# Kernel tuning notes

Measured on AMD Instinct MI355X. Metric: run time of the kernel, lower is better.

The kernel has to match this reference:

```python
import jax, jax.numpy as jnp
import numpy as np

HIDDEN = 2048
HEAD_DIM = 128
Q_HEAD = 16
KV_HEAD = 2
MAX_TOKEN = 4096
THETA = 10000
B = 1
S = 2048
SCALER = 1.0 / np.sqrt(HEAD_DIM)


def make_pos_emb():
    # Faithful port of ROPEEmbedding.create_embedding
    i = np.repeat(np.arange(HEAD_DIM // 2), 2)            # [D]
    freq = np.power(float(THETA), -i * 2.0 / HEAD_DIM)    # [D]
    t = np.einsum('i,j->ij', freq, np.arange(MAX_TOKEN, dtype=np.float64))  # [D, T]
    cos = np.cos(t)
    sin = np.sin(t)
    sin[0::2] *= -1.0                                      # negate even rows (even dim indices)
    pe = np.concatenate([cos, sin], axis=0).T              # [T, 2D]
    return jnp.asarray(pe, jnp.float32)


def _flip_pairs(x):
    # swap adjacent pairs along last dim: (x0,x1,x2,x3,..) -> (x1,x0,x3,x2,..)
    b, h, s, d = x.shape
    return x.reshape(b, h, s, d // 2, 2)[..., ::-1].reshape(b, h, s, d)


def _apply_rope(x, pos_emb):
    # x: [B, H, S, D]; pos_emb: [max_token, 2D]
    s = x.shape[2]
    pe = pos_emb[:s]                     # [S, 2D]
    cos = pe[:, :HEAD_DIM]               # [S, D]
    sin = pe[:, HEAD_DIM:]               # [S, D] (signed)
    return x * cos + _flip_pairs(x) * sin


def setup_inputs() -> dict:
    key = jax.random.key(0)
    ks = jax.random.split(key, 5)
    qkv_out = (Q_HEAD + 2 * KV_HEAD) * HEAD_DIM  # 2560
    lim_qkv = 1.0 / np.sqrt(HIDDEN)
    lim_o = 1.0 / np.sqrt(Q_HEAD * HEAD_DIM)
    x = jax.random.normal(ks[0], (B, S, HIDDEN), dtype=jnp.float32)
    w_qkv = jax.random.uniform(ks[1], (qkv_out, HIDDEN), jnp.float32, -lim_qkv, lim_qkv)
    b_qkv = jax.random.uniform(ks[2], (qkv_out,), jnp.float32, -lim_qkv, lim_qkv)
    w_o = jax.random.uniform(ks[3], (HIDDEN, Q_HEAD * HEAD_DIM), jnp.float32, -lim_o, lim_o)
    b_o = jax.random.uniform(ks[4], (HIDDEN,), jnp.float32, -lim_o, lim_o)
    # causal additive mask, as typically passed to this module
    neg = jnp.float32(-1e9)
    attention_mask = jnp.where(
        jnp.tril(jnp.ones((S, S), dtype=bool)), jnp.float32(0.0), neg
    )[None, None, :, :]
    pos_emb = make_pos_emb()
    return {"tensor": x, "attention_mask": attention_mask, "w_qkv": w_qkv,
            "b_qkv": b_qkv, "w_o": w_o, "b_o": b_o, "pos_emb": pos_emb}


def reference(tensor, attention_mask, w_qkv, b_qkv, w_o, b_o, pos_emb):
    b, s, _ = tensor.shape
    qkv = tensor @ w_qkv.T + b_qkv                        # [B, S, 2560]
    dq = HEAD_DIM * Q_HEAD
    dkv = HEAD_DIM * KV_HEAD
    q = qkv[..., :dq].reshape(b, s, Q_HEAD, HEAD_DIM)
    k = qkv[..., dq:dq + dkv].reshape(b, s, KV_HEAD, HEAD_DIM)
    v = qkv[..., dq + dkv:].reshape(b, s, KV_HEAD, HEAD_DIM)
    scale = Q_HEAD // KV_HEAD
    k = jnp.repeat(k, scale, axis=2)                      # [B, S, Q_HEAD, D]
    v = jnp.repeat(v, scale, axis=2)
    q = q.transpose(0, 2, 1, 3)                           # [B, H, S, D]
    k = k.transpose(0, 2, 1, 3)
    v = v.transpose(0, 2, 1, 3)
    q = _apply_rope(q, pos_emb)
    k = _apply_rope(k, pos_emb)
    scores = jnp.einsum('bhqd,bhkd->bhqk', q, k) * SCALER
    scores = scores + attention_mask
    attn = jax.nn.softmax(scores, axis=-1)
    out = jnp.einsum('bhqk,bhkd->bhqd', attn, v)          # [B, H, S, D]
    out = out.transpose(0, 2, 1, 3).reshape(b, s, Q_HEAD * HEAD_DIM)
    return out @ w_o.T + b_o
```

## Files before the change

### kernel.cpp

```cpp
#include <hip/hip_runtime.h>
#include <stdint.h>

#define SQ 2048
#define DH 128
#define SCALER 0.08838834764831845f

typedef float f32x4 __attribute__((ext_vector_type(4)));
typedef short s16x8 __attribute__((ext_vector_type(8)));
typedef short s16x4 __attribute__((ext_vector_type(4)));

__device__ __forceinline__ short f2bf(float f) {
  uint32_t x = __float_as_uint(f);
  uint32_t r = (x + 0x7fffu + ((x >> 16) & 1u)) >> 16;
  return (short)(r & 0xffffu);
}

__device__ __forceinline__ void mfma16(f32x4& d, s16x8 a, s16x8 b) {
  asm("v_mfma_f32_16x16x32_bf16 %0, %1, %2, %0" : "+v"(d) : "v"(a), "v"(b));
}

__device__ __forceinline__ void gload16(const void* g, void* l) {
  __builtin_amdgcn_global_load_lds(
      (__attribute__((address_space(1))) void*)const_cast<void*>(g),
      (__attribute__((address_space(3))) void*)l, 16, 0, 0);
}

__global__ __launch_bounds__(256) void cvt3_bf16(
    const float* __restrict__ a, const float* __restrict__ b,
    const float* __restrict__ c, short* __restrict__ out,
    int na8, int nb8, int nc8) {
  int i = blockIdx.x * 256 + threadIdx.x;
  if (i >= na8 + nb8 + nc8) return;
  const float* src;
  if (i < na8) src = a + (size_t)i * 8;
  else if (i < na8 + nb8) src = b + (size_t)(i - na8) * 8;
  else src = c + (size_t)(i - na8 - nb8) * 8;
  const float4* p = (const float4*)src;
  float4 u = p[0], v = p[1];
  s16x8 o;
  o[0] = f2bf(u.x); o[1] = f2bf(u.y); o[2] = f2bf(u.z); o[3] = f2bf(u.w);
  o[4] = f2bf(v.x); o[5] = f2bf(v.y); o[6] = f2bf(v.z); o[7] = f2bf(v.w);
  *((s16x8*)out + i) = o;
}

template <int MODE>
__global__ __launch_bounds__(256) void gemm_bt_bias(
    const short* __restrict__ A, const short* __restrict__ B,
    const float* __restrict__ bias, float* __restrict__ C,
    const float* __restrict__ pe, short* __restrict__ qws,
    short* __restrict__ kws, short* __restrict__ vtws,
    int M, int N, int K) {
  __shared__ __align__(16) short As_[2][128 * 64];
  __shared__ __align__(16) short Bs_[2][64 * 64];
  const int t = threadIdx.x;
  const int l = t & 63, w = t >> 6;
  const int wr = w >> 1, wc = w & 1;
  const int lr = l & 15, lk = l >> 4;
  const int m0 = blockIdx.y * 128, n0 = blockIdx.x * 64;

  f32x4 acc[4][2] = {};

#define GSTAGE(buf, kt)                                                         \
  {                                                                             \
    const short* ga = A + (size_t)m0 * K + (kt);                                \
    const short* gb = B + (size_t)n0 * K + (kt);                                \
    _Pragma("unroll") for (int i = 0; i < 4; ++i) {                             \
      int j = i * 256 + t;                                                      \
      int lbase = (i * 256 + (t & ~63)) << 4;                                   \
      gload16(ga + (size_t)(j >> 3) * K + ((j & 7) << 3),                       \
              (char*)As_[buf] + lbase);                                         \
    }                                                                           \
    _Pragma("unroll") for (int i = 0; i < 2; ++i) {                             \
      int j = i * 256 + t;                                                      \
      int lbase = (i * 256 + (t & ~63)) << 4;                                   \
      gload16(gb + (size_t)(j >> 3) * K + ((j & 7) << 3),                       \
              (char*)Bs_[buf] + lbase);                                         \
    }                                                                           \
  }

  GSTAGE(0, 0);
  __syncthreads();

  const int nk = K >> 6;
  for (int ki = 0; ki < nk; ++ki) {
    const int cur = ki & 1;
    if (ki + 1 < nk) GSTAGE(cur ^ 1, (ki + 1) << 6);
    const short* As = As_[cur];
    const short* Bs = Bs_[cur];
#pragma unroll
    for (int ks = 0; ks < 2; ++ks) {
      s16x8 af[4], bg[2];
#pragma unroll
      for (int i = 0; i < 4; ++i)
        af[i] = *(const s16x8*)(As + (wr * 64 + i * 16 + lr) * 64 + ks * 32 + lk * 8);
#pragma unroll
      for (int i = 0; i < 2; ++i)
        bg[i] = *(const s16x8*)(Bs + (wc * 32 + i * 16 + lr) * 64 + ks * 32 + lk * 8);
#pragma unroll
      for (int mi = 0; mi < 4; ++mi)
#pragma unroll
        for (int ni = 0; ni < 2; ++ni)
          mfma16(acc[mi][ni], af[mi], bg[ni]);
    }
    __syncthreads();
  }
#undef GSTAGE

  if (MODE == 0) {
#pragma unroll
    for (int mi = 0; mi < 4; ++mi) {
      int row = m0 + wr * 64 + mi * 16 + lk * 4;
#pragma unroll
      for (int ni = 0; ni < 2; ++ni) {
        int col = n0 + wc * 32 + ni * 16 + lr;
        float bv = bias[col];
#pragma unroll
        for (int r = 0; r < 4; ++r)
          C[(size_t)(row + r) * N + col] = acc[mi][ni][r] + bv;
      }
    }
  } else {
    short* Ct = (short*)As_;
    if (n0 < 2304) {
#pragma unroll
      for (int mi = 0; mi < 4; ++mi) {
        int row_l = wr * 64 + mi * 16 + lk * 4;
#pragma unroll
        for (int ni = 0; ni < 2; ++ni) {
          int col_l = wc * 32 + ni * 16 + lr;
          int col = n0 + col_l;
          float bv = bias[col];
          int d = col & 127;
#pragma unroll
          for (int r = 0; r < 4; ++r) {
            float v = acc[mi][ni][r] + bv;
            float p = __shfl_xor(v, 1);
            int s = m0 + row_l + r;
            const float* per = pe + (size_t)s * 256;
            float y = v * per[d] + p * per[128 + d];
            if (n0 < 2048) y *= SCALER;
            Ct[(row_l + r) * 72 + col_l] = f2bf(y);
          }
        }
      }
      __syncthreads();
      if (n0 < 2048) {
        int hq = n0 >> 7, d0 = n0 & 127;
#pragma unroll
        for (int i = 0; i < 4; ++i) {
          int idx = i * 256 + t;
          int sl = idx >> 3, c = idx & 7;
          s16x8 val = *(const s16x8*)(Ct + sl * 72 + c * 8);
          *(s16x8*)(qws + ((size_t)hq * SQ + m0 + sl) * DH + d0 + c * 8) = val;
        }
      } else {
        int hk = (n0 - 2048) >> 7, d0 = (n0 - 2048) & 127;
#pragma unroll
        for (int i = 0; i < 4; ++i) {
          int idx = i * 256 + t;
          int sl = idx >> 3, c = idx & 7;
          s16x8 val = *(const s16x8*)(Ct + sl * 72 + c * 8);
          int slot = ((d0 >> 3) + c) ^ (sl & 15);
          *(s16x8*)(kws + (size_t)hk * SQ * DH + (size_t)(m0 + sl) * DH + slot * 8) = val;
        }
      }
    } else {
      int hk = (n0 - 2304) >> 7, d0 = (n0 - 2304) & 127;
#pragma unroll
      for (int mi = 0; mi < 4; ++mi) {
        int row_l = wr * 64 + mi * 16 + lk * 4;
#pragma unroll
        for (int ni = 0; ni < 2; ++ni) {
          int col_l = wc * 32 + ni * 16 + lr;
          float bv = bias[n0 + col_l];
#pragma unroll
          for (int r = 0; r < 4; ++r)
            Ct[col_l * 136 + row_l + r] = f2bf(acc[mi][ni][r] + bv);
        }
      }
      __syncthreads();
#pragma unroll
      for (int i = 0; i < 4; ++i) {
        int idx = i * 256 + t;
        int dl = idx >> 4, c = idx & 15;
        s16x8 val = *(const s16x8*)(Ct + dl * 136 + c * 8);
        int d = d0 + dl;
        size_t dst = (size_t)hk * DH * SQ + (size_t)d * SQ +
                     (size_t)((m0 >> 6) + (c >> 3)) * 64 +
                     (size_t)(((c & 7) ^ (d & 7)) << 3);
        *(s16x8*)(vtws + dst) = val;
      }
    }
  }
}

__global__ __launch_bounds__(256) void attn_fwd(
    const short* __restrict__ qws, const short* __restrict__ kws,
    const short* __restrict__ vtws, short* __restrict__ attnws) {
  __shared__ __align__(16) short Ks[2][64 * 128];
  __shared__ __align__(16) short Vt[2][128 * 64];
  __shared__ __align__(16) short Ps[4][16 * 72];

  const int bx = blockIdx.x;
  const int h = bx & 15;
  const int i_ = bx >> 4;
  const int qb = (i_ < 16) ? (31 - i_) : (i_ - 16);
  const int hk = h >> 3;
  const int t = threadIdx.x, l = t & 63, w = t >> 6;
  const int lr = l & 15, lk = l >> 4;

  s16x8 qf[4];
  {
    const short* qbase = qws + ((size_t)h * SQ + (size_t)qb * 64 + w * 16) * DH;
#pragma unroll
    for (int kd = 0; kd < 4; ++kd)
      qf[kd] = *(const s16x8*)(qbase + (size_t)lr * DH + kd * 32 + lk * 8);
  }

  f32x4 o[8] = {};
  float m_ = -1e30f, l_ = 0.f;

  const short* gkh = kws + (size_t)hk * SQ * DH;
  const short* gvh = vtws + (size_t)hk * DH * SQ;

#define STAGE(buf, kb)                                                          \
  {                                                                             \
    const short* gk = gkh + (size_t)(kb)*64 * DH;                               \
    const short* gv = gvh + (size_t)(kb)*64;                                    \
    _Pragma("unroll") for (int i = 0; i < 4; ++i) {                             \
      int j = i * 256 + t;                                                      \
      int lbase = (i * 256 + (t & ~63)) << 4;                                   \
      gload16(gk + (size_t)(j >> 4) * DH + ((j & 15) << 3),                     \
              (char*)Ks[buf] + lbase);                                          \
      gload16(gv + (size_t)(j >> 3) * SQ + ((j & 7) << 3),                      \
              (char*)Vt[buf] + lbase);                                          \
    }                                                                           \
  }

  STAGE(0, 0);
  __syncthreads();

  for (int kb = 0; kb <= qb; ++kb) {
    const int cur = kb & 1;
    if (kb < qb) STAGE(cur ^ 1, kb + 1);

    f32x4 sc_[4] = {};
#pragma unroll
    for (int kd = 0; kd < 4; ++kd) {
#pragma unroll
      for (int nt = 0; nt < 4; ++nt) {
        int krow = nt * 16 + lr;
        int slot = (kd * 4 + lk) ^ lr;
        s16x8 kf = *(const s16x8*)(Ks[cur] + krow * 128 + slot * 8);
        mfma16(sc_[nt], kf, qf[kd]);
      }
    }
    if (kb == qb) {
      int qloc = w * 16 + lr;
#pragma unroll
      for (int nt = 0; nt < 4; ++nt)
#pragma unroll
        for (int r = 0; r < 4; ++r) {
          int col = nt * 16 + lk * 4 + r;
          if (col > qloc) sc_[nt][r] = -1e30f;
        }
    }
    {
      float rm = -1e30f;
#pragma unroll
      for (int nt = 0; nt < 4; ++nt)
        rm = fmaxf(rm, fmaxf(fmaxf(sc_[nt][0], sc_[nt][1]),
                             fmaxf(sc_[nt][2], sc_[nt][3])));
      rm = fmaxf(rm, __shfl_xor(rm, 16));
      rm = fmaxf(rm, __shfl_xor(rm, 32));
      float mn = fmaxf(m_, rm);
      float scl = __expf(m_ - mn);
      float rs = 0.f;
#pragma unroll
      for (int nt = 0; nt < 4; ++nt)
#pragma unroll
        for (int r = 0; r < 4; ++r) {
          sc_[nt][r] = __expf(sc_[nt][r] - mn);
          rs += sc_[nt][r];
        }
      rs += __shfl_xor(rs, 16);
      rs += __shfl_xor(rs, 32);
      l_ = l_ * scl + rs;
      m_ = mn;
#pragma unroll
      for (int dt = 0; dt < 8; ++dt)
#pragma unroll
        for (int r = 0; r < 4; ++r) o[dt][r] *= scl;
    }
    {
      short* ps = (short*)Ps[w];
#pragma unroll
      for (int nt = 0; nt < 4; ++nt)
#pragma unroll
        for (int r = 0; r < 4; ++r)
          ps[lr * 72 + nt * 16 + lk * 4 + r] = f2bf(sc_[nt][r]);
    }
    {
      const short* ps = (const short*)Ps[w];
#pragma unroll
      for (int kp = 0; kp < 2; ++kp) {
        s16x8 pbf = *(const s16x8*)(ps + lr * 72 + kp * 32 + lk * 8);
#pragma unroll
        for (int dt = 0; dt < 8; ++dt) {
          int drow = dt * 16 + lr;
          int slot = (kp * 4 + lk) ^ (lr & 7);
          s16x8 vb = *(const s16x8*)(Vt[cur] + drow * 64 + slot * 8);
          mfma16(o[dt], vb, pbf);
        }
      }
    }
    __syncthreads();
  }
#undef STAGE

  {
    int srow = qb * 64 + w * 16 + lr;
#pragma unroll
    for (int dt = 0; dt < 8; ++dt) {
      s16x4 st;
#pragma unroll
      for (int r = 0; r < 4; ++r) st[r] = f2bf(o[dt][r] / l_);
      *(s16x4*)(attnws + (size_t)srow * 2048 + h * DH + dt * 16 + lk * 4) = st;
    }
  }
}

extern "C" void kernel_launch(void* const* d_in, const int* in_sizes, int n_in,
                              void* d_out, int out_size, void* d_ws, size_t ws_size,
                              hipStream_t stream) {
  (void)in_sizes; (void)n_in; (void)out_size; (void)ws_size;
  const float* x     = (const float*)d_in[0];
  const float* w_qkv = (const float*)d_in[2];
  const float* b_qkv = (const float*)d_in[3];
  const float* w_o   = (const float*)d_in[4];
  const float* b_o   = (const float*)d_in[5];
  const float* pe    = (const float*)d_in[6];
  float* out = (float*)d_out;

  short* xb     = (short*)d_ws;
  short* wqkvb  = xb + (size_t)2048 * 2048;
  short* wob    = wqkvb + (size_t)2560 * 2048;
  short* qws    = wob + (size_t)2048 * 2048;
  short* kws    = qws + (size_t)16 * 2048 * 128;
  short* vtws   = kws + (size_t)2 * 2048 * 128;
  short* attnws = vtws + (size_t)2 * 128 * 2048;

  cvt3_bf16<<<6656, 256, 0, stream>>>(x, w_qkv, w_o, xb,
                                      2048 * 2048 / 8, 2560 * 2048 / 8, 2048 * 2048 / 8);
  gemm_bt_bias<1><<<dim3(2560 / 64, 2048 / 128), 256, 0, stream>>>(
      xb, wqkvb, b_qkv, nullptr, pe, qws, kws, vtws, 2048, 2560, 2048);
  attn_fwd<<<512, 256, 0, stream>>>(qws, kws, vtws, attnws);
  gemm_bt_bias<0><<<dim3(2048 / 64, 2048 / 128), 256, 0, stream>>>(
      attnws, wob, b_o, out, nullptr, nullptr, nullptr, nullptr, 2048, 2048, 2048);
}
```

Baseline: 149.0 us.

## Read K/V directly from global memory, add lazy softmax rescale and MFMA priority

Removes the double-buffered LDS staging of K and V tiles and the per-iteration block barrier, so each wave reads its K and pre-swizzled V^T fragments straight from global memory (relying on L1/L2 caching). Adds a lazy online-softmax rescale that skips updating the running max and rescaling the accumulator when the new row max exceeds the old by at most 8. Also raises wave priority around the MFMA loops. This removes LDS traffic and synchronisation but exposes global-load latency and redundant loads across the four waves. The skip threshold risks larger exponents, though they stay bounded by e^8.

```diff
diff --git a/kernel.cpp b/kernel.cpp
--- a/kernel.cpp
+++ b/kernel.cpp
@@ -197,8 +197,6 @@
 __global__ __launch_bounds__(256) void attn_fwd(
     const short* __restrict__ qws, const short* __restrict__ kws,
     const short* __restrict__ vtws, short* __restrict__ attnws) {
-  __shared__ __align__(16) short Ks[2][64 * 128];
-  __shared__ __align__(16) short Vt[2][128 * 64];
   __shared__ __align__(16) short Ps[4][16 * 72];
 
   const int bx = blockIdx.x;
@@ -223,38 +221,23 @@
   const short* gkh = kws + (size_t)hk * SQ * DH;
   const short* gvh = vtws + (size_t)hk * DH * SQ;
 
-#define STAGE(buf, kb)                                                          \
-  {                                                                             \
-    const short* gk = gkh + (size_t)(kb)*64 * DH;                               \
-    const short* gv = gvh + (size_t)(kb)*64;                                    \
-    _Pragma("unroll") for (int i = 0; i < 4; ++i) {                             \
-      int j = i * 256 + t;                                                      \
-      int lbase = (i * 256 + (t & ~63)) << 4;                                   \
-      gload16(gk + (size_t)(j >> 4) * DH + ((j & 15) << 3),                     \
-              (char*)Ks[buf] + lbase);                                          \
-      gload16(gv + (size_t)(j >> 3) * SQ + ((j & 7) << 3),                      \
-              (char*)Vt[buf] + lbase);                                          \
-    }                                                                           \
-  }
-
-  STAGE(0, 0);
-  __syncthreads();
-
   for (int kb = 0; kb <= qb; ++kb) {
-    const int cur = kb & 1;
-    if (kb < qb) STAGE(cur ^ 1, kb + 1);
+    const short* kbase = gkh + (size_t)kb * 64 * DH;
+    const short* vbase = gvh + (size_t)kb * 64;
 
     f32x4 sc_[4] = {};
+    __builtin_amdgcn_s_setprio(1);
 #pragma unroll
     for (int kd = 0; kd < 4; ++kd) {
 #pragma unroll
       for (int nt = 0; nt < 4; ++nt) {
         int krow = nt * 16 + lr;
         int slot = (kd * 4 + lk) ^ lr;
-        s16x8 kf = *(const s16x8*)(Ks[cur] + krow * 128 + slot * 8);
+        s16x8 kf = *(const s16x8*)(kbase + (size_t)krow * DH + slot * 8);
         mfma16(sc_[nt], kf, qf[kd]);
       }
     }
+    __builtin_amdgcn_s_setprio(0);
     if (kb == qb) {
       int qloc = w * 16 + lr;
 #pragma unroll
@@ -273,8 +256,8 @@
                              fmaxf(sc_[nt][2], sc_[nt][3])));
       rm = fmaxf(rm, __shfl_xor(rm, 16));
       rm = fmaxf(rm, __shfl_xor(rm, 32));
-      float mn = fmaxf(m_, rm);
-      float scl = __expf(m_ - mn);
+      const bool skip = __all(rm - m_ <= 8.0f);
+      const float mn = skip ? m_ : fmaxf(m_, rm);
       float rs = 0.f;
 #pragma unroll
       for (int nt = 0; nt < 4; ++nt)
@@ -285,12 +268,17 @@
         }
       rs += __shfl_xor(rs, 16);
       rs += __shfl_xor(rs, 32);
-      l_ = l_ * scl + rs;
-      m_ = mn;
-#pragma unroll
-      for (int dt = 0; dt < 8; ++dt)
-#pragma unroll
-        for (int r = 0; r < 4; ++r) o[dt][r] *= scl;
+      if (skip) {
+        l_ += rs;
+      } else {
+        float scl = __expf(m_ - mn);
+        l_ = l_ * scl + rs;
+        m_ = mn;
+#pragma unroll
+        for (int dt = 0; dt < 8; ++dt)
+#pragma unroll
+          for (int r = 0; r < 4; ++r) o[dt][r] *= scl;
+      }
     }
     {
       short* ps = (short*)Ps[w];
@@ -302,6 +290,7 @@
     }
     {
       const short* ps = (const short*)Ps[w];
+      __builtin_amdgcn_s_setprio(1);
 #pragma unroll
       for (int kp = 0; kp < 2; ++kp) {
         s16x8 pbf = *(const s16x8*)(ps + lr * 72 + kp * 32 + lk * 8);
@@ -309,14 +298,13 @@
         for (int dt = 0; dt < 8; ++dt) {
           int drow = dt * 16 + lr;
           int slot = (kp * 4 + lk) ^ (lr & 7);
-          s16x8 vb = *(const s16x8*)(Vt[cur] + drow * 64 + slot * 8);
+          s16x8 vb = *(const s16x8*)(vbase + (size_t)drow * SQ + slot * 8);
           mfma16(o[dt], vb, pbf);
         }
       }
-    }
-    __syncthreads();
-  }
-#undef STAGE
+      __builtin_amdgcn_s_setprio(0);
+    }
+  }
 
   {
     int srow = qb * 64 + w * 16 + lr;
```

After: 289.8 us. 1.94x slower.
